# Optimization experiments

Hardware: AMD Instinct MI355X
Metric: run time of the kernel (lower is better)

The kernel has to match this reference:

```python
import jax, jax.numpy as jnp
import numpy as np
from jax import lax

HUMAN_CONF = 0.7
IOU_TH = 0.5


def setup_inputs() -> dict:
    key = jax.random.key(0)
    k1, k2 = jax.random.split(key)
    B, Q, C = 16, 2048, 2
    return {
        "human_logits": jax.random.normal(k1, (B, Q, C), dtype=jnp.float32),
        "pred_boxes": jax.random.uniform(k2, (B, Q, 4), dtype=jnp.float32),  # cxcywh in [0,1]
        "img_h": 800,
        "img_w": 1333,
    }


def box_cxcywh_to_xyxy(b):
    cx, cy, w, h = b[..., 0], b[..., 1], b[..., 2], b[..., 3]
    return jnp.stack([cx - 0.5 * w, cy - 0.5 * h, cx + 0.5 * w, cy + 0.5 * h], axis=-1)


def pairwise_iou(b):
    # b: [Q,4] xyxy -> iou: [Q,Q]
    area = jnp.clip(b[:, 2] - b[:, 0], 0) * jnp.clip(b[:, 3] - b[:, 1], 0)
    lt = jnp.maximum(b[:, None, :2], b[None, :, :2])
    rb = jnp.minimum(b[:, None, 2:], b[None, :, 2:])
    wh = jnp.clip(rb - lt, 0)
    inter = wh[..., 0] * wh[..., 1]
    union = area[:, None] + area[None, :] - inter
    return inter / jnp.maximum(union, 1e-9)


def nms_keep(boxes, scores, valid, iou_th):
    # Greedy NMS on one image with fixed shapes; returns keep mask [Q].
    Q = scores.shape[0]
    order = jnp.argsort(jnp.where(valid, -scores, jnp.inf))  # valid boxes first, score desc
    b = boxes[order]
    v = valid[order]
    iou = pairwise_iou(b)                       # [Q,Q]
    idx = jnp.arange(Q)
    sup_mat = (iou > iou_th) & (idx[None, :] > idx[:, None])  # i suppresses later j

    def step(supp, i):
        keep_i = v[i] & jnp.logical_not(supp[i])
        supp = supp | (keep_i & sup_mat[i])
        return supp, keep_i

    _, keep_sorted = lax.scan(step, jnp.zeros(Q, bool), idx)
    return jnp.zeros(Q, bool).at[order].set(keep_sorted)


def reference(human_logits, pred_boxes, img_h, img_w):
    prob = jax.nn.softmax(human_logits, axis=-1)          # [B,Q,C]
    scores = prob.max(axis=-1)                            # [B,Q]
    labels = prob.argmax(axis=-1)                         # [B,Q]
    boxes = box_cxcywh_to_xyxy(pred_boxes)                # [B,Q,4]
    scale = jnp.array([img_w, img_h, img_w, img_h], dtype=boxes.dtype)
    boxes = boxes * scale
    valid = (labels == 0) & (scores >= HUMAN_CONF)
    keep = jax.vmap(lambda b, s, v: nms_keep(b, s, v, IOU_TH))(boxes, scores, valid)
    scores_out = jnp.where(keep, scores, 0.0)
    boxes_out = jnp.where(keep[..., None], boxes, 0.0).astype(jnp.int32)
    return scores_out, boxes_out, keep
```

## Files before the change

### kernel.cpp

```cpp
#include <hip/hip_runtime.h>
#include <math.h>


#define QN    2048
#define NS    1024
#define MATW  17408
#define MAGIC 0x5ca1ab1eu

__device__ __forceinline__ int rb32(int wb) { return 64 * wb * (33 - wb); }

__device__ __forceinline__ unsigned long long shfl_xor_u64(unsigned long long x, int m) {
    int lo = __shfl_xor((int)(unsigned)(x & 0xffffffffull), m, 64);
    int hi = __shfl_xor((int)(unsigned)(x >> 32), m, 64);
    return ((unsigned long long)(unsigned)hi << 32) | (unsigned)lo;
}

__device__ __forceinline__ unsigned long long score_key(float2 l, int q, bool* valid_out) {
    float mx = fmaxf(l.x, l.y), mn = fminf(l.x, l.y);
    float e = expf(mn - mx);
    float score = 1.0f / (1.0f + e);
    bool valid = (l.x >= l.y) && (score >= 0.7f);
    *valid_out = valid;
    unsigned sbits = valid ? __float_as_uint(score) : 0u;
    return ((unsigned long long)(~sbits) << 32) | (unsigned)q;
}

__global__ __launch_bounds__(1024, 4) void kfused(
    const float* __restrict__ logits, const float* __restrict__ pboxes,
    const int* __restrict__ img_h_p, const int* __restrict__ img_w_p,
    unsigned* __restrict__ wflag, unsigned* __restrict__ wmat,
    float* __restrict__ out, int B)
{
    __shared__ __align__(16) char smem[41216];
    unsigned long long* skey = (unsigned long long*)smem;
    float* sx1 = (float*)(smem + 8192);
    float* sy1 = (float*)(smem + 12288);
    float* sx2 = (float*)(smem + 16384);
    float* sy2 = (float*)(smem + 20480);
    float* sar = (float*)(smem + 24576);
    unsigned short* sidxl = (unsigned short*)(smem + 28672);
    unsigned char* keepq = (unsigned char*)(smem + 30720);
    unsigned* skm = (unsigned*)(smem + 32768);
    int* sMp = (int*)(smem + 32896);
    unsigned long long* skeyB = (unsigned long long*)(smem + 33024);

    const int blk = blockIdx.x;
    const int b = blk % B, slice = blk / B;
    const int tid = threadIdx.x, lane = tid & 63, wave = tid >> 6;
    const float sw = (float)(*img_w_p), sh = (float)(*img_h_p);

    if (tid == 0) *sMp = 0;
    keepq[tid] = 0; keepq[tid + 1024] = 0;
    if (tid < 32) skm[tid] = 0;
    __syncthreads();

    const unsigned long long lmask_lt = (1ull << lane) - 1ull;
#pragma unroll
    for (int qq = 0; qq < 2; ++qq) {
        int q = tid + qq * 1024;
        float2 l = ((const float2*)logits)[b * QN + q];
        bool valid;
        unsigned long long key = score_key(l, q, &valid);
        unsigned long long mb = __ballot(valid);
        int base = 0;
        if (lane == 0 && mb) base = atomicAdd(sMp, __popcll(mb));
        base = __shfl(base, 0, 64);
        if (valid) {
            int slot = base + __popcll(mb & lmask_lt);
            if (slot < NS) skey[slot] = key;
        }
    }
    __syncthreads();
    const int M = *sMp;

    if (M <= NS) {
        unsigned long long v = (tid < M) ? skey[tid] : ~0ull;
        __syncthreads();
#pragma unroll
        for (int k = 2; k <= 64; k <<= 1) {
            bool dir = ((tid & k) == 0);
#pragma unroll
            for (int j = k >> 1; j > 0; j >>= 1) {
                unsigned long long o = shfl_xor_u64(v, j);
                bool takeMin = (dir == ((tid & j) == 0));
                v = ((v < o) == takeMin) ? v : o;
            }
        }
        int pp = 0;
        for (int k = 128; k <= NS; k <<= 1) {
            bool dir = ((tid & k) == 0);
            for (int j = k >> 1; j >= 64; j >>= 1) {
                unsigned long long* buf = pp ? skeyB : skey;
                pp ^= 1;
                buf[tid] = v;
                __syncthreads();
                unsigned long long o = buf[tid ^ j];
                bool takeMin = (dir == ((tid & j) == 0));
                v = ((v < o) == takeMin) ? v : o;
            }
#pragma unroll
            for (int j = 32; j > 0; j >>= 1) {
                unsigned long long o = shfl_xor_u64(v, j);
                bool takeMin = (dir == ((tid & j) == 0));
                v = ((v < o) == takeMin) ? v : o;
            }
        }
        int qi = (int)((unsigned)v & 0xffffu);
        sidxl[tid] = (unsigned short)qi;
        float x1 = 0.f, y1 = 0.f, x2 = 0.f, y2 = 0.f, ar = 0.f;
        if (tid < M) {
            float4 pb = ((const float4*)pboxes)[b * QN + qi];
            x1 = (pb.x - 0.5f * pb.z) * sw;
            y1 = (pb.y - 0.5f * pb.w) * sh;
            x2 = (pb.x + 0.5f * pb.z) * sw;
            y2 = (pb.y + 0.5f * pb.w) * sh;
            ar = fmaxf(x2 - x1, 0.f) * fmaxf(y2 - y1, 0.f);
        }
        sx1[tid] = x1; sy1[tid] = y1; sx2[tid] = x2; sy2[tid] = y2; sar[tid] = ar;
        __syncthreads();

        unsigned* mat = wmat + (long)b * MATW;
        const int NG = (M + 3) >> 2;
        const int W64 = (M + 63) >> 6;
        for (int gi = slice * 16 + wave; gi < NG; gi += 128) {
            const int g = gi << 2;
            const int nr = min(4, M - g);
            const int wb = g >> 6;
            const int rl = 32 - 2 * wb;
            float ax1[4], ay1[4], ax2[4], ay2[4], aar[4];
            int rbase[4];
#pragma unroll
            for (int r = 0; r < 4; ++r) {
                int i = g + min(r, nr - 1);
                ax1[r] = sx1[i]; ay1[r] = sy1[i];
                ax2[r] = sx2[i]; ay2[r] = sy2[i]; aar[r] = sar[i];
                rbase[r] = rb32(wb) + ((g + r) & 63) * rl;
            }
            for (int w = wb; w < W64; ++w) {
                int j = (w << 6) | lane;
                float bx1 = sx1[j], by1 = sy1[j], bx2 = sx2[j], by2 = sy2[j], bar = sar[j];
#pragma unroll
                for (int r = 0; r < 4; ++r) {
                    float ltx = fmaxf(ax1[r], bx1), lty = fmaxf(ay1[r], by1);
                    float rbx = fminf(ax2[r], bx2), rby = fminf(ay2[r], by2);
                    float wx = fmaxf(rbx - ltx, 0.f), wy = fmaxf(rby - lty, 0.f);
                    float inter = wx * wy;
                    float uni = aar[r] + bar - inter;
                    float iou = inter / fmaxf(uni, 1e-9f);
                    bool sup = (iou > 0.5f) && (j > g + r);
                    unsigned long long bal = __ballot(sup);
                    if (lane == 0 && r < nr)
                        *(unsigned long long*)(mat + rbase[r] + 2 * (w - wb)) = bal;
                }
            }
        }
        __syncthreads();
        if (tid == 0)
            __hip_atomic_store(&wflag[b * 8 + slice], MAGIC,
                               __ATOMIC_RELEASE, __HIP_MEMORY_SCOPE_AGENT);
        if (slice != 0) return;

        if (wave == 0) {
            const unsigned* fp = &wflag[b * 8 + (lane & 7)];
            for (;;) {
                unsigned f = (lane < 8)
                    ? __hip_atomic_load(fp, __ATOMIC_ACQUIRE, __HIP_MEMORY_SCOPE_AGENT)
                    : MAGIC;
                if (__all(f == MAGIC)) break;
                __builtin_amdgcn_s_sleep(2);
            }
            const unsigned* gm = wmat + (long)b * MATW;
            unsigned rem = 0;
            const int Ms = __builtin_amdgcn_readfirstlane(M);
            const int C = (Ms + 31) >> 5;
            unsigned rcur[32], rnxt[32];
            if (C > 0) {
                int Lc = min(tid, 31);
#pragma unroll
                for (int t = 0; t < 32; ++t) rcur[t] = gm[Lc + t * 32];
            }
            for (int c = 0; c < C; ++c) {
                if (c + 1 < C) {
                    int cn = c + 1, wbn = cn >> 1, rln = 32 - 2 * wbn;
                    int Lcn = min(max(tid, 2 * wbn), 31);
                    int rb0n = rb32(wbn) + ((cn & 1) << 5) * rln + (Lcn - 2 * wbn);
#pragma unroll
                    for (int t = 0; t < 32; ++t) rnxt[t] = gm[rb0n + t * rln];
                }
                unsigned rw = (unsigned)__builtin_amdgcn_readlane((int)rem, c);
                unsigned keepmask = 0;
                int lim = min(32, Ms - (c << 5));
#pragma unroll
                for (int t = 0; t < 32; ++t) {
                    if (t < lim && !((rw >> t) & 1u)) {
                        keepmask |= (1u << t);
                        rem |= rcur[t];
                        rw |= (unsigned)__builtin_amdgcn_readlane((int)rcur[t], c);
                    }
                }
                if (tid == 0) skm[c] = keepmask;
                if (c + 1 < C) {
#pragma unroll
                    for (int t = 0; t < 32; ++t) rcur[t] = rnxt[t];
                }
            }
        }
        __syncthreads();
        for (int s = tid; s < M; s += 1024)
            if ((skm[s >> 5] >> (s & 31)) & 1u) keepq[sidxl[s]] = 1;
        __syncthreads();
    } else {
        if (slice != 0) return;
        unsigned long long* skeyF = (unsigned long long*)smem;
        unsigned char* ssupp = (unsigned char*)(smem + 16384);
        for (int q = tid; q < QN; q += 1024) {
            float2 l = ((const float2*)logits)[b * QN + q];
            bool valid;
            skeyF[q] = score_key(l, q, &valid);
        }
        __syncthreads();
        for (int k = 2; k <= QN; k <<= 1)
            for (int j = k >> 1; j > 0; j >>= 1) {
                int i = ((tid & ~(j - 1)) << 1) | (tid & (j - 1));
                int p = i | j;
                bool up = ((i & k) == 0);
                unsigned long long a = skeyF[i], c2 = skeyF[p];
                if ((a > c2) == up) { skeyF[i] = c2; skeyF[p] = a; }
                __syncthreads();
            }
        for (int s = tid; s < M; s += 1024) ssupp[s] = 0;
        __syncthreads();
        for (int i = 0; i < M; ++i) {
            __syncthreads();
            if (ssupp[i]) continue;
            int ia = (unsigned short)(unsigned)skeyF[i];
            float4 pa = ((const float4*)pboxes)[b * QN + ia];
            float ax1 = (pa.x - 0.5f * pa.z) * sw, ay1 = (pa.y - 0.5f * pa.w) * sh;
            float ax2 = (pa.x + 0.5f * pa.z) * sw, ay2 = (pa.y + 0.5f * pa.w) * sh;
            float areaA = fmaxf(ax2 - ax1, 0.f) * fmaxf(ay2 - ay1, 0.f);
            for (int jj = i + 1 + tid; jj < M; jj += 1024) {
                int jb = (unsigned short)(unsigned)skeyF[jj];
                float4 pq = ((const float4*)pboxes)[b * QN + jb];
                float bx1 = (pq.x - 0.5f * pq.z) * sw, by1 = (pq.y - 0.5f * pq.w) * sh;
                float bx2 = (pq.x + 0.5f * pq.z) * sw, by2 = (pq.y + 0.5f * pq.w) * sh;
                float ltx = fmaxf(ax1, bx1), lty = fmaxf(ay1, by1);
                float rbx = fminf(ax2, bx2), rby = fminf(ay2, by2);
                float wx = fmaxf(rbx - ltx, 0.f), wy = fmaxf(rby - lty, 0.f);
                float inter = wx * wy;
                float areaB = fmaxf(bx2 - bx1, 0.f) * fmaxf(by2 - by1, 0.f);
                float uni = areaA + areaB - inter;
                if (inter / fmaxf(uni, 1e-9f) > 0.5f) ssupp[jj] = 1;
            }
        }
        __syncthreads();
        for (int s = tid; s < M; s += 1024)
            if (!ssupp[s]) keepq[(unsigned short)(unsigned)skeyF[s]] = 1;
        __syncthreads();
    }

    const long BQ = (long)B * QN;
#pragma unroll
    for (int qq = 0; qq < 2; ++qq) {
        int q = tid + qq * 1024;
        int base = b * QN + q;
        float2 l = ((const float2*)logits)[base];
        float e = expf(fminf(l.x, l.y) - fmaxf(l.x, l.y));
        float score = 1.0f / (1.0f + e);
        float4 pb = ((const float4*)pboxes)[base];
        float x1 = (pb.x - 0.5f * pb.z) * sw, y1 = (pb.y - 0.5f * pb.w) * sh;
        float x2 = (pb.x + 0.5f * pb.z) * sw, y2 = (pb.y + 0.5f * pb.w) * sh;
        int kp = keepq[q];
        out[base] = kp ? score : 0.f;
        out[BQ * 5 + base] = kp ? 1.f : 0.f;
        float4 ob;
        ob.x = kp ? truncf(x1) : 0.f;
        ob.y = kp ? truncf(y1) : 0.f;
        ob.z = kp ? truncf(x2) : 0.f;
        ob.w = kp ? truncf(y2) : 0.f;
        ((float4*)(out + BQ))[base] = ob;
    }
}

extern "C" void kernel_launch(void* const* d_in, const int* in_sizes, int n_in,
                              void* d_out, int out_size, void* d_ws, size_t ws_size,
                              hipStream_t stream) {
    const float* logits = (const float*)d_in[0];
    const float* pboxes = (const float*)d_in[1];
    const int*   img_h  = (const int*)d_in[2];
    const int*   img_w  = (const int*)d_in[3];
    float* out = (float*)d_out;
    const int B = in_sizes[0] / (QN * 2);

    char* ws = (char*)d_ws;
    unsigned* wflag = (unsigned*)(ws + 0);
    unsigned* wmat  = (unsigned*)(ws + 1024);

    kfused<<<dim3(B * 8), dim3(1024), 0, stream>>>(logits, pboxes, img_h, img_w,
                                                   wflag, wmat, out, B);
}
```

Before: 102.3 us.

## Split mask build over 16 slices, stage mask in LDS, write only kept outputs

```diff
diff --git a/kernel.cpp b/kernel.cpp
--- a/kernel.cpp
+++ b/kernel.cpp
@@ -2,10 +2,11 @@
 #include <math.h>
 
 
-#define QN    2048
-#define NS    1024
-#define MATW  17408
-#define MAGIC 0x5ca1ab1eu
+#define QN     2048
+#define NS     1024
+#define NSLICE 16
+#define MATW   17408
+#define MAGIC  0x5ca1ab1eu
 
 __device__ __forceinline__ int rb32(int wb) { return 64 * wb * (33 - wb); }
 
@@ -25,13 +26,13 @@
     return ((unsigned long long)(~sbits) << 32) | (unsigned)q;
 }
 
-__global__ __launch_bounds__(1024, 4) void kfused(
+__global__ __launch_bounds__(1024) void kfused(
     const float* __restrict__ logits, const float* __restrict__ pboxes,
     const int* __restrict__ img_h_p, const int* __restrict__ img_w_p,
     unsigned* __restrict__ wflag, unsigned* __restrict__ wmat,
     float* __restrict__ out, int B)
 {
-    __shared__ __align__(16) char smem[41216];
+    __shared__ __align__(16) char smem[110848];
     unsigned long long* skey = (unsigned long long*)smem;
     float* sx1 = (float*)(smem + 8192);
     float* sy1 = (float*)(smem + 12288);
@@ -39,19 +40,18 @@
     float* sy2 = (float*)(smem + 20480);
     float* sar = (float*)(smem + 24576);
     unsigned short* sidxl = (unsigned short*)(smem + 28672);
-    unsigned char* keepq = (unsigned char*)(smem + 30720);
-    unsigned* skm = (unsigned*)(smem + 32768);
     int* sMp = (int*)(smem + 32896);
     unsigned long long* skeyB = (unsigned long long*)(smem + 33024);
+    unsigned* skm = (unsigned*)(smem + 33024);
+    unsigned* smat = (unsigned*)(smem + 41216);
 
     const int blk = blockIdx.x;
     const int b = blk % B, slice = blk / B;
     const int tid = threadIdx.x, lane = tid & 63, wave = tid >> 6;
     const float sw = (float)(*img_w_p), sh = (float)(*img_h_p);
+    const long BQ = (long)B * QN;
 
     if (tid == 0) *sMp = 0;
-    keepq[tid] = 0; keepq[tid + 1024] = 0;
-    if (tid < 32) skm[tid] = 0;
     __syncthreads();
 
     const unsigned long long lmask_lt = (1ull << lane) - 1ull;
@@ -122,7 +122,7 @@
         unsigned* mat = wmat + (long)b * MATW;
         const int NG = (M + 3) >> 2;
         const int W64 = (M + 63) >> 6;
-        for (int gi = slice * 16 + wave; gi < NG; gi += 128) {
+        for (int gi = slice * 16 + wave; gi < NG; gi += 256) {
             const int g = gi << 2;
             const int nr = min(4, M - g);
             const int wb = g >> 6;
@@ -154,70 +154,107 @@
                 }
             }
         }
-        __syncthreads();
-        if (tid == 0)
-            __hip_atomic_store(&wflag[b * 8 + slice], MAGIC,
-                               __ATOMIC_RELEASE, __HIP_MEMORY_SCOPE_AGENT);
-        if (slice != 0) return;
-
-        if (wave == 0) {
-            const unsigned* fp = &wflag[b * 8 + (lane & 7)];
-            for (;;) {
-                unsigned f = (lane < 8)
-                    ? __hip_atomic_load(fp, __ATOMIC_ACQUIRE, __HIP_MEMORY_SCOPE_AGENT)
-                    : MAGIC;
-                if (__all(f == MAGIC)) break;
-                __builtin_amdgcn_s_sleep(2);
-            }
-            const unsigned* gm = wmat + (long)b * MATW;
+    }
+
+    if (tid < 128) {
+        int q = slice * 128 + tid;
+        int base = b * QN + q;
+        out[base] = 0.f;
+        out[BQ * 5 + base] = 0.f;
+        float4 z; z.x = 0.f; z.y = 0.f; z.z = 0.f; z.w = 0.f;
+        ((float4*)(out + BQ))[base] = z;
+    }
+
+    __syncthreads();
+    if (tid == 0)
+        __hip_atomic_store(&wflag[b * NSLICE + slice], MAGIC,
+                           __ATOMIC_RELEASE, __HIP_MEMORY_SCOPE_AGENT);
+    if (slice != 0) return;
+
+    if (wave == 0) {
+        const unsigned* fp = &wflag[b * NSLICE + (lane & (NSLICE - 1))];
+        for (;;) {
+            unsigned f = (lane < NSLICE)
+                ? __hip_atomic_load(fp, __ATOMIC_ACQUIRE, __HIP_MEMORY_SCOPE_AGENT)
+                : MAGIC;
+            if (__all(f == MAGIC)) break;
+            __builtin_amdgcn_s_sleep(2);
+        }
+    }
+    __syncthreads();
+
+    if (M <= NS) {
+        const int W64 = (M + 63) >> 6;
+        const int nw4 = rb32(W64) >> 2;
+        const uint4* gm4 = (const uint4*)(wmat + (long)b * MATW);
+        uint4* sm4 = (uint4*)smat;
+        for (int i = tid; i < nw4; i += 1024) sm4[i] = gm4[i];
+        __syncthreads();
+
+        if (tid < 64) {
+            const unsigned* gm = smat;
             unsigned rem = 0;
             const int Ms = __builtin_amdgcn_readfirstlane(M);
             const int C = (Ms + 31) >> 5;
-            unsigned rcur[32], rnxt[32];
-            if (C > 0) {
-                int Lc = min(tid, 31);
-#pragma unroll
-                for (int t = 0; t < 32; ++t) rcur[t] = gm[Lc + t * 32];
-            }
+            const int lam = min(tid, 31);
+            unsigned rcur[32];
             for (int c = 0; c < C; ++c) {
-                if (c + 1 < C) {
-                    int cn = c + 1, wbn = cn >> 1, rln = 32 - 2 * wbn;
-                    int Lcn = min(max(tid, 2 * wbn), 31);
-                    int rb0n = rb32(wbn) + ((cn & 1) << 5) * rln + (Lcn - 2 * wbn);
-#pragma unroll
-                    for (int t = 0; t < 32; ++t) rnxt[t] = gm[rb0n + t * rln];
+                const int wb = c >> 1, rl = 32 - 2 * wb;
+                const int half = (c & 1) << 5;
+                const int Lc = min(max(tid, 2 * wb), 31);
+                const int rb0 = rb32(wb) + half * rl + (Lc - 2 * wb);
+#pragma unroll
+                for (int t = 0; t < 32; ++t) rcur[t] = gm[rb0 + t * rl];
+                unsigned diag = gm[rb32(wb) + (half + lam) * rl + (c - 2 * wb)];
+
+                int lim = min(32, Ms - (c << 5));
+                unsigned limmask = (lim >= 32) ? 0xFFFFFFFFu : ((1u << lim) - 1u);
+                unsigned rw = ((unsigned)__builtin_amdgcn_readlane((int)rem, c))
+                              | ~limmask;
+                unsigned keepmask = 0;
+#pragma unroll
+                for (int t = 0; t < 32; ++t) {
+                    unsigned keep = ((~rw) >> t) & 1u;
+                    unsigned rword = (unsigned)__builtin_amdgcn_readlane((int)diag, t);
+                    rw |= (0u - keep) & rword;
+                    keepmask |= keep << t;
                 }
-                unsigned rw = (unsigned)__builtin_amdgcn_readlane((int)rem, c);
-                unsigned keepmask = 0;
-                int lim = min(32, Ms - (c << 5));
-#pragma unroll
-                for (int t = 0; t < 32; ++t) {
-                    if (t < lim && !((rw >> t) & 1u)) {
-                        keepmask |= (1u << t);
-                        rem |= rcur[t];
-                        rw |= (unsigned)__builtin_amdgcn_readlane((int)rcur[t], c);
-                    }
-                }
+#pragma unroll
+                for (int t = 0; t < 32; ++t)
+                    rem |= (0u - ((keepmask >> t) & 1u)) & rcur[t];
                 if (tid == 0) skm[c] = keepmask;
-                if (c + 1 < C) {
-#pragma unroll
-                    for (int t = 0; t < 32; ++t) rcur[t] = rnxt[t];
-                }
-            }
-        }
-        __syncthreads();
-        for (int s = tid; s < M; s += 1024)
-            if ((skm[s >> 5] >> (s & 31)) & 1u) keepq[sidxl[s]] = 1;
-        __syncthreads();
+            }
+        }
+        __syncthreads();
+
+        for (int s = tid; s < M; s += 1024) {
+            if ((skm[s >> 5] >> (s & 31)) & 1u) {
+                int qi = sidxl[s];
+                int base = b * QN + qi;
+                float2 l = ((const float2*)logits)[base];
+                float e = expf(fminf(l.x, l.y) - fmaxf(l.x, l.y));
+                float score = 1.0f / (1.0f + e);
+                float4 pb = ((const float4*)pboxes)[base];
+                float x1 = (pb.x - 0.5f * pb.z) * sw, y1 = (pb.y - 0.5f * pb.w) * sh;
+                float x2 = (pb.x + 0.5f * pb.z) * sw, y2 = (pb.y + 0.5f * pb.w) * sh;
+                out[base] = score;
+                out[BQ * 5 + base] = 1.f;
+                float4 ob;
+                ob.x = truncf(x1); ob.y = truncf(y1);
+                ob.z = truncf(x2); ob.w = truncf(y2);
+                ((float4*)(out + BQ))[base] = ob;
+            }
+        }
     } else {
-        if (slice != 0) return;
         unsigned long long* skeyF = (unsigned long long*)smem;
         unsigned char* ssupp = (unsigned char*)(smem + 16384);
-        for (int q = tid; q < QN; q += 1024) {
-            float2 l = ((const float2*)logits)[b * QN + q];
+        unsigned char* keepqF = (unsigned char*)(smem + 18432);
+        for (int qq = tid; qq < QN; qq += 1024) {
+            float2 l = ((const float2*)logits)[b * QN + qq];
             bool valid;
-            skeyF[q] = score_key(l, q, &valid);
-        }
+            skeyF[qq] = score_key(l, qq, &valid);
+        }
+        keepqF[tid] = 0; keepqF[tid + 1024] = 0;
         __syncthreads();
         for (int k = 2; k <= QN; k <<= 1)
             for (int j = k >> 1; j > 0; j >>= 1) {
@@ -254,30 +291,28 @@
         }
         __syncthreads();
         for (int s = tid; s < M; s += 1024)
-            if (!ssupp[s]) keepq[(unsigned short)(unsigned)skeyF[s]] = 1;
-        __syncthreads();
-    }
-
-    const long BQ = (long)B * QN;
-#pragma unroll
-    for (int qq = 0; qq < 2; ++qq) {
-        int q = tid + qq * 1024;
-        int base = b * QN + q;
-        float2 l = ((const float2*)logits)[base];
-        float e = expf(fminf(l.x, l.y) - fmaxf(l.x, l.y));
-        float score = 1.0f / (1.0f + e);
-        float4 pb = ((const float4*)pboxes)[base];
-        float x1 = (pb.x - 0.5f * pb.z) * sw, y1 = (pb.y - 0.5f * pb.w) * sh;
-        float x2 = (pb.x + 0.5f * pb.z) * sw, y2 = (pb.y + 0.5f * pb.w) * sh;
-        int kp = keepq[q];
-        out[base] = kp ? score : 0.f;
-        out[BQ * 5 + base] = kp ? 1.f : 0.f;
-        float4 ob;
-        ob.x = kp ? truncf(x1) : 0.f;
-        ob.y = kp ? truncf(y1) : 0.f;
-        ob.z = kp ? truncf(x2) : 0.f;
-        ob.w = kp ? truncf(y2) : 0.f;
-        ((float4*)(out + BQ))[base] = ob;
+            if (!ssupp[s]) keepqF[(unsigned short)(unsigned)skeyF[s]] = 1;
+        __syncthreads();
+#pragma unroll
+        for (int qq = 0; qq < 2; ++qq) {
+            int q = tid + qq * 1024;
+            int base = b * QN + q;
+            float2 l = ((const float2*)logits)[base];
+            float e = expf(fminf(l.x, l.y) - fmaxf(l.x, l.y));
+            float score = 1.0f / (1.0f + e);
+            float4 pb = ((const float4*)pboxes)[base];
+            float x1 = (pb.x - 0.5f * pb.z) * sw, y1 = (pb.y - 0.5f * pb.w) * sh;
+            float x2 = (pb.x + 0.5f * pb.z) * sw, y2 = (pb.y + 0.5f * pb.w) * sh;
+            int kp = keepqF[q];
+            out[base] = kp ? score : 0.f;
+            out[BQ * 5 + base] = kp ? 1.f : 0.f;
+            float4 ob;
+            ob.x = kp ? truncf(x1) : 0.f;
+            ob.y = kp ? truncf(y1) : 0.f;
+            ob.z = kp ? truncf(x2) : 0.f;
+            ob.w = kp ? truncf(y2) : 0.f;
+            ((float4*)(out + BQ))[base] = ob;
+        }
     }
 }
 
@@ -295,6 +330,6 @@
     unsigned* wflag = (unsigned*)(ws + 0);
     unsigned* wmat  = (unsigned*)(ws + 1024);
 
-    kfused<<<dim3(B * 8), dim3(1024), 0, stream>>>(logits, pboxes, img_h, img_w,
-                                                   wflag, wmat, out, B);
+    kfused<<<dim3(B * NSLICE), dim3(1024), 0, stream>>>(logits, pboxes, img_h, img_w,
+                                                        wflag, wmat, out, B);
 }
```

Result: faster. 97.13 us (-5.0%).
